# Optimization experiments

Measured on AMD Instinct MI355X. Metric: run time of the kernel, lower is better.

Reference implementation:

```python
import jax, jax.numpy as jnp
import numpy as np

N, P, D = 8, 4096, 3


def _chamfer_one_direction(x, y, x_lengths, y_lengths):
    # x: (N,P1,D), y: (N,P2,D); squared-L2 k=1 NN of each x point in y (norm=2 in knn_points)
    P1 = x.shape[1]
    P2 = y.shape[1]
    x2 = jnp.sum(x * x, axis=-1)  # (N,P1)
    y2 = jnp.sum(y * y, axis=-1)  # (N,P2)
    d2 = x2[:, :, None] + y2[:, None, :] - 2.0 * jnp.einsum('npd,nqd->npq', x, y)  # (N,P1,P2)
    # mask padded y points out of the NN search
    y_mask = jnp.arange(P2)[None, :] >= y_lengths[:, None]  # (N,P2) True = padded
    d2 = jnp.where(y_mask[:, None, :], jnp.inf, d2)
    cham = jnp.min(d2, axis=2)  # (N,P1) dist to nearest valid y
    # zero out padded x points
    x_mask = jnp.arange(P1)[None, :] >= x_lengths[:, None]  # (N,P1)
    cham = jnp.where(x_mask, 0.0, cham)
    # point_reduction='mean'
    per_cloud = jnp.sum(cham, axis=1) / jnp.maximum(x_lengths, 1).astype(x.dtype)  # (N,)
    # batch_reduction='mean' (no weights -> divide by N)
    return jnp.sum(per_cloud) / x.shape[0]


def setup_inputs() -> dict:
    key = jax.random.key(0)
    k1, k2, k3, k4 = jax.random.split(key, 4)
    x = jax.random.normal(k1, (N, P, D), dtype=jnp.float32)
    y = jax.random.normal(k2, (N, P, D), dtype=jnp.float32)
    x_lengths = jax.random.randint(k3, (N,), P // 2, P + 1)
    y_lengths = jax.random.randint(k4, (N,), P // 2, P + 1)
    return {"x": x, "y": y, "x_lengths": x_lengths, "y_lengths": y_lengths}


def reference(x, y, x_lengths, y_lengths):
    cham_x = _chamfer_one_direction(x, y, x_lengths, y_lengths)
    cham_y = _chamfer_one_direction(y, x, y_lengths, x_lengths)
    return cham_x + cham_y
```

## Files before the change

### kernel.cpp

```cpp
#include <hip/hip_runtime.h>
#include <hip/hip_bf16.h>
#include <math.h>

constexpr int NB  = 8;
constexpr int PP  = 4096;

constexpr int TPB = 256;
constexpr int XPT = 8;
constexpr int XCH = TPB * XPT;
constexpr int NXC = PP / XCH;
constexpr int NYC = 32;
constexpr int YCH = PP / NYC;

constexpr int NSEG = 4;
constexpr int SEGP = PP / NSEG;
constexpr int NPART = 2 * NB * NSEG;

__global__ __launch_bounds__(TPB, 4) void nn_partial(
    const float* __restrict__ x, const float* __restrict__ y,
    const int* __restrict__ xlen, const int* __restrict__ ylen,
    float* __restrict__ ws)
{
    __shared__ float4 sy[YCH];

    int bid = blockIdx.x;
    const int yc  = bid & (NYC - 1); bid >>= 5;
    const int xc  = bid & (NXC - 1); bid >>= 1;
    const int n   = bid & (NB - 1);  bid >>= 3;
    const int dir = bid;

    const float* __restrict__ xs = dir ? y : x;
    const float* __restrict__ ys = dir ? x : y;
    const int yl = (dir ? xlen : ylen)[n];

    float m0[XPT], m1[XPT], m2[XPT], a[XPT], emin[XPT];
    const int xi0 = xc * XCH + (int)threadIdx.x;
    const float* __restrict__ xb = xs + (size_t)n * PP * 3;
#pragma unroll
    for (int k = 0; k < XPT; ++k) {
        int xi = xi0 + k * TPB;
        float x0 = xb[xi * 3 + 0];
        float x1 = xb[xi * 3 + 1];
        float x2 = xb[xi * 3 + 2];
        m0[k] = -2.f * x0; m1[k] = -2.f * x1; m2[k] = -2.f * x2;
        a[k]  = fmaf(x0, x0, fmaf(x1, x1, x2 * x2));
        emin[k] = INFINITY;
    }

    const float* __restrict__ ybase = ys + ((size_t)n * PP + (size_t)yc * YCH) * 3;
    if ((int)threadIdx.x < YCH) {
        int p = (int)threadIdx.x;
        float y0 = ybase[p * 3 + 0];
        float y1 = ybase[p * 3 + 1];
        float y2 = ybase[p * 3 + 2];
        sy[p] = make_float4(y0, y1, y2, fmaf(y0, y0, fmaf(y1, y1, y2 * y2)));
    }
    __syncthreads();

    int jend = yl - yc * YCH;
    if (jend > YCH) jend = YCH;

#pragma unroll 4
    for (int j = 0; j < jend; ++j) {
        float4 v = sy[j];
#pragma unroll
        for (int k = 0; k < XPT; ++k) {
            float e = fmaf(m0[k], v.x, fmaf(m1[k], v.y, fmaf(m2[k], v.z, v.w)));
            emin[k] = fminf(emin[k], e);
        }
    }

    float* __restrict__ w = ws + ((size_t)(dir * NB + n) * NYC + yc) * PP;
#pragma unroll
    for (int k = 0; k < XPT; ++k) {
        int xi = xi0 + k * TPB;
        w[xi] = a[k] + emin[k];
    }
}

__global__ __launch_bounds__(256) void reduce_cloud(
    const float* __restrict__ ws,
    const int* __restrict__ xlen, const int* __restrict__ ylen,
    float* __restrict__ partial)
{
    const int b   = blockIdx.x;
    const int seg = b & (NSEG - 1);
    const int c   = b >> 2;
    const int dir = c >> 3;
    const int n   = c & (NB - 1);
    const int xl  = (dir ? ylen : xlen)[n];

    const float* __restrict__ w = ws + (size_t)c * NYC * PP;
    float sum = 0.f;
    const int i0 = seg * SEGP;
    for (int i = i0 + (int)threadIdx.x; i < i0 + SEGP; i += 256) {
        float m = w[i];
#pragma unroll
        for (int ch = 1; ch < NYC; ++ch) m = fminf(m, w[(size_t)ch * PP + i]);
        if (i < xl) sum += m;
    }

#pragma unroll
    for (int off = 32; off > 0; off >>= 1) sum += __shfl_xor(sum, off);
    __shared__ float ls[4];
    const int lane = (int)threadIdx.x & 63;
    const int wv   = (int)threadIdx.x >> 6;
    if (lane == 0) ls[wv] = sum;
    __syncthreads();
    if (threadIdx.x == 0) {
        float tot = ls[0] + ls[1] + ls[2] + ls[3];
        int d = xl > 1 ? xl : 1;
        partial[b] = tot / (float)d / (float)NB;
    }
}

__global__ __launch_bounds__(64) void final_sum(
    const float* __restrict__ partial, float* __restrict__ out)
{
    float v = partial[threadIdx.x];
#pragma unroll
    for (int off = 32; off > 0; off >>= 1) v += __shfl_xor(v, off);
    if (threadIdx.x == 0) out[0] = v;
}

__global__ __launch_bounds__(TPB) void chamfer_atomic(
    const float* __restrict__ x, const float* __restrict__ y,
    const int* __restrict__ xlen, const int* __restrict__ ylen,
    float* __restrict__ out)
{
    __shared__ float4 sy[YCH];

    int bid = blockIdx.x;
    const int xc  = bid & (NXC - 1); bid >>= 1;
    const int n   = bid & (NB - 1);  bid >>= 3;
    const int dir = bid;

    const float* __restrict__ xs = dir ? y : x;
    const float* __restrict__ ys = dir ? x : y;
    const int yl = (dir ? xlen : ylen)[n];
    const int xl = (dir ? ylen : xlen)[n];

    float m0[XPT], m1[XPT], m2[XPT], a[XPT], emin[XPT];
    const int xi0 = xc * XCH + (int)threadIdx.x;
    const float* __restrict__ xb = xs + (size_t)n * PP * 3;
#pragma unroll
    for (int k = 0; k < XPT; ++k) {
        int xi = xi0 + k * TPB;
        float x0 = xb[xi * 3 + 0];
        float x1 = xb[xi * 3 + 1];
        float x2 = xb[xi * 3 + 2];
        m0[k] = -2.f * x0; m1[k] = -2.f * x1; m2[k] = -2.f * x2;
        a[k]  = fmaf(x0, x0, fmaf(x1, x1, x2 * x2));
        emin[k] = INFINITY;
    }

    for (int yc = 0; yc < NYC; ++yc) {
        const float* __restrict__ ybase = ys + ((size_t)n * PP + (size_t)yc * YCH) * 3;
        __syncthreads();
        if ((int)threadIdx.x < YCH) {
            int p = (int)threadIdx.x;
            float y0 = ybase[p * 3 + 0];
            float y1 = ybase[p * 3 + 1];
            float y2 = ybase[p * 3 + 2];
            sy[p] = make_float4(y0, y1, y2, fmaf(y0, y0, fmaf(y1, y1, y2 * y2)));
        }
        __syncthreads();
        int jend = yl - yc * YCH;
        if (jend > YCH) jend = YCH;
#pragma unroll 4
        for (int j = 0; j < jend; ++j) {
            float4 v = sy[j];
#pragma unroll
            for (int k = 0; k < XPT; ++k) {
                float e = fmaf(m0[k], v.x, fmaf(m1[k], v.y, fmaf(m2[k], v.z, v.w)));
                emin[k] = fminf(emin[k], e);
            }
        }
    }

    float sum = 0.f;
#pragma unroll
    for (int k = 0; k < XPT; ++k) {
        int xi = xi0 + k * TPB;
        if (xi < xl) sum += a[k] + emin[k];
    }
#pragma unroll
    for (int off = 32; off > 0; off >>= 1) sum += __shfl_xor(sum, off);
    __shared__ float ls[4];
    const int lane = (int)threadIdx.x & 63;
    const int wv   = (int)threadIdx.x >> 6;
    if (lane == 0) ls[wv] = sum;
    __syncthreads();
    if (threadIdx.x == 0) {
        float tot = ls[0] + ls[1] + ls[2] + ls[3];
        int d = xl > 1 ? xl : 1;
        atomicAdd(out, tot / (float)d / (float)NB);
    }
}

extern "C" void kernel_launch(void* const* d_in, const int* in_sizes, int n_in,
                              void* d_out, int out_size, void* d_ws, size_t ws_size,
                              hipStream_t stream) {
    const float* x  = (const float*)d_in[0];
    const float* y  = (const float*)d_in[1];
    const int* xl   = (const int*)d_in[2];
    const int* yl   = (const int*)d_in[3];
    float* out      = (float*)d_out;

    const size_t ws_floats = (size_t)2 * NB * NYC * PP;
    const size_t ws_need   = (ws_floats + NPART) * sizeof(float);

    if (ws_size >= ws_need) {
        float* ws      = (float*)d_ws;
        float* partial = ws + ws_floats;
        const int gridA = 2 * NB * NXC * NYC;
        nn_partial<<<gridA, TPB, 0, stream>>>(x, y, xl, yl, ws);
        reduce_cloud<<<NPART, 256, 0, stream>>>(ws, xl, yl, partial);
        final_sum<<<1, 64, 0, stream>>>(partial, out);
    } else {
        hipMemsetAsync(d_out, 0, sizeof(float), stream);
        const int gridF = 2 * NB * NXC;
        chamfer_atomic<<<gridF, TPB, 0, stream>>>(x, y, xl, yl, out);
    }
}
```

Measured before the change: 33.82 us.

## Fold final sum into reduce kernel, shuffle block order, skip padded query waves

Removes the separate final_sum launch by having the last reduce block, found with an atomic counter, sum the partials itself. The block index is scrambled with a multiplier so that y-chunks of different lengths are spread evenly across CUs. Each wave now owns a contiguous run of x points, so a wave whose points all lie past the query length skips its NN loop. The -2 factor moves onto the y side in shared memory, and the inner loop handles two y points per step. The counter reset inside the first kernel relies on stream ordering, and the skipped waves write garbage values that reduce_cloud then masks out.

New measurement: 56.99 us. 68.5% more time.

```diff
diff --git a/kernel.cpp b/kernel.cpp
--- a/kernel.cpp
+++ b/kernel.cpp
@@ -11,6 +11,7 @@
 constexpr int NXC = PP / XCH;
 constexpr int NYC = 32;
 constexpr int YCH = PP / NYC;
+constexpr int GRIDA = 2 * NB * NXC * NYC;
 
 constexpr int NSEG = 4;
 constexpr int SEGP = PP / NSEG;
@@ -19,69 +20,88 @@
 __global__ __launch_bounds__(TPB, 4) void nn_partial(
     const float* __restrict__ x, const float* __restrict__ y,
     const int* __restrict__ xlen, const int* __restrict__ ylen,
-    float* __restrict__ ws)
+    float* __restrict__ ws, unsigned int* __restrict__ counter)
 {
     __shared__ float4 sy[YCH];
 
-    int bid = blockIdx.x;
-    const int yc  = bid & (NYC - 1); bid >>= 5;
-    const int xc  = bid & (NXC - 1); bid >>= 1;
-    const int n   = bid & (NB - 1);  bid >>= 3;
-    const int dir = bid;
+    if (blockIdx.x == 0 && threadIdx.x == 0) atomicExch(counter, 0u);
+
+    const int item = ((int)blockIdx.x * 331) & (GRIDA - 1);
+    const int yc  = item & (NYC - 1);
+    const int xc  = (item >> 5) & (NXC - 1);
+    const int n   = (item >> 6) & (NB - 1);
+    const int dir = (item >> 9) & 1;
 
     const float* __restrict__ xs = dir ? y : x;
     const float* __restrict__ ys = dir ? x : y;
     const int yl = (dir ? xlen : ylen)[n];
-
-    float m0[XPT], m1[XPT], m2[XPT], a[XPT], emin[XPT];
-    const int xi0 = xc * XCH + (int)threadIdx.x;
+    const int ql = (dir ? ylen : xlen)[n];
+
+    const float* __restrict__ yb = ys + ((size_t)n * PP + (size_t)yc * YCH) * 3;
+    if ((int)threadIdx.x < YCH) {
+        const int p = (int)threadIdx.x;
+        float y0 = yb[p * 3 + 0];
+        float y1 = yb[p * 3 + 1];
+        float y2 = yb[p * 3 + 2];
+        sy[p] = make_float4(-2.f * y0, -2.f * y1, -2.f * y2,
+                            fmaf(y0, y0, fmaf(y1, y1, y2 * y2)));
+    }
+
+    const int wave  = (int)threadIdx.x >> 6;
+    const int lane  = (int)threadIdx.x & 63;
+    const int wbase = xc * XCH + wave * (XPT * 64);
+
+    float px0[XPT], px1[XPT], px2[XPT], a[XPT], emin[XPT];
     const float* __restrict__ xb = xs + (size_t)n * PP * 3;
 #pragma unroll
     for (int k = 0; k < XPT; ++k) {
-        int xi = xi0 + k * TPB;
-        float x0 = xb[xi * 3 + 0];
-        float x1 = xb[xi * 3 + 1];
-        float x2 = xb[xi * 3 + 2];
-        m0[k] = -2.f * x0; m1[k] = -2.f * x1; m2[k] = -2.f * x2;
-        a[k]  = fmaf(x0, x0, fmaf(x1, x1, x2 * x2));
+        const int xi = wbase + k * 64 + lane;
+        px0[k] = xb[xi * 3 + 0];
+        px1[k] = xb[xi * 3 + 1];
+        px2[k] = xb[xi * 3 + 2];
+        a[k]   = fmaf(px0[k], px0[k], fmaf(px1[k], px1[k], px2[k] * px2[k]));
         emin[k] = INFINITY;
-    }
-
-    const float* __restrict__ ybase = ys + ((size_t)n * PP + (size_t)yc * YCH) * 3;
-    if ((int)threadIdx.x < YCH) {
-        int p = (int)threadIdx.x;
-        float y0 = ybase[p * 3 + 0];
-        float y1 = ybase[p * 3 + 1];
-        float y2 = ybase[p * 3 + 2];
-        sy[p] = make_float4(y0, y1, y2, fmaf(y0, y0, fmaf(y1, y1, y2 * y2)));
     }
     __syncthreads();
 
     int jend = yl - yc * YCH;
     if (jend > YCH) jend = YCH;
 
-#pragma unroll 4
-    for (int j = 0; j < jend; ++j) {
-        float4 v = sy[j];
-#pragma unroll
-        for (int k = 0; k < XPT; ++k) {
-            float e = fmaf(m0[k], v.x, fmaf(m1[k], v.y, fmaf(m2[k], v.z, v.w)));
-            emin[k] = fminf(emin[k], e);
+    if (ql > wbase && jend > 0) {
+        const int j2 = jend & ~1;
+#pragma unroll 2
+        for (int j = 0; j < j2; j += 2) {
+            const float4 u = sy[j];
+            const float4 v = sy[j + 1];
+#pragma unroll
+            for (int k = 0; k < XPT; ++k) {
+                float e1 = fmaf(px0[k], u.x, fmaf(px1[k], u.y, fmaf(px2[k], u.z, u.w)));
+                float e2 = fmaf(px0[k], v.x, fmaf(px1[k], v.y, fmaf(px2[k], v.z, v.w)));
+                emin[k] = fminf(emin[k], fminf(e1, e2));
+            }
+        }
+        if (jend & 1) {
+            const float4 u = sy[jend - 1];
+#pragma unroll
+            for (int k = 0; k < XPT; ++k) {
+                float e1 = fmaf(px0[k], u.x, fmaf(px1[k], u.y, fmaf(px2[k], u.z, u.w)));
+                emin[k] = fminf(emin[k], e1);
+            }
         }
     }
 
     float* __restrict__ w = ws + ((size_t)(dir * NB + n) * NYC + yc) * PP;
 #pragma unroll
     for (int k = 0; k < XPT; ++k) {
-        int xi = xi0 + k * TPB;
-        w[xi] = a[k] + emin[k];
+        w[wbase + k * 64 + lane] = a[k] + emin[k];
     }
 }
 
 __global__ __launch_bounds__(256) void reduce_cloud(
     const float* __restrict__ ws,
     const int* __restrict__ xlen, const int* __restrict__ ylen,
-    float* __restrict__ partial)
+    float* __restrict__ partial, unsigned int* __restrict__ counter,
+    float* __restrict__ out)
 {
     const int b   = blockIdx.x;
     const int seg = b & (NSEG - 1);
@@ -111,16 +131,16 @@
         float tot = ls[0] + ls[1] + ls[2] + ls[3];
         int d = xl > 1 ? xl : 1;
         partial[b] = tot / (float)d / (float)NB;
-    }
-}
-
-__global__ __launch_bounds__(64) void final_sum(
-    const float* __restrict__ partial, float* __restrict__ out)
-{
-    float v = partial[threadIdx.x];
-#pragma unroll
-    for (int off = 32; off > 0; off >>= 1) v += __shfl_xor(v, off);
-    if (threadIdx.x == 0) out[0] = v;
+        __threadfence();
+        unsigned int old = atomicAdd(counter, 1u);
+        if (old == NPART - 1) {
+            __threadfence();
+            float s = 0.f;
+            for (int i = 0; i < NPART; ++i)
+                s += atomicAdd(&partial[i], 0.0f);
+            out[0] = s;
+        }
+    }
 }
 
 __global__ __launch_bounds__(TPB) void chamfer_atomic(
@@ -208,15 +228,14 @@
     float* out      = (float*)d_out;
 
     const size_t ws_floats = (size_t)2 * NB * NYC * PP;
-    const size_t ws_need   = (ws_floats + NPART) * sizeof(float);
+    const size_t ws_need   = (ws_floats + NPART + 1) * sizeof(float);
 
     if (ws_size >= ws_need) {
-        float* ws      = (float*)d_ws;
-        float* partial = ws + ws_floats;
-        const int gridA = 2 * NB * NXC * NYC;
-        nn_partial<<<gridA, TPB, 0, stream>>>(x, y, xl, yl, ws);
-        reduce_cloud<<<NPART, 256, 0, stream>>>(ws, xl, yl, partial);
-        final_sum<<<1, 64, 0, stream>>>(partial, out);
+        float* ws            = (float*)d_ws;
+        float* partial       = ws + ws_floats;
+        unsigned int* counter = (unsigned int*)(partial + NPART);
+        nn_partial<<<GRIDA, TPB, 0, stream>>>(x, y, xl, yl, ws, counter);
+        reduce_cloud<<<NPART, 256, 0, stream>>>(ws, xl, yl, partial, counter, out);
     } else {
         hipMemsetAsync(d_out, 0, sizeof(float), stream);
         const int gridF = 2 * NB * NXC;
```
